# Kernel optimization log

Measured on AMD Instinct MI355X. Metric: run time of the kernel, lower is better.

## Reference

```python
import jax, jax.numpy as jnp
import numpy as np

B, I, O = 4096, 2048, 2048
U_R, THR_MIN = 0.01, 0.01


def setup_inputs() -> dict:
    key = jax.random.key(0)
    ks = jax.random.split(key, 4)
    # Random small-scale weights (the module's ones-init saturates sigmoids;
    # math is identical, this just keeps values in a testable range).
    return {
        "x_t": jax.random.normal(ks[0], (B, I), jnp.float32),
        "u_t": jnp.zeros((B, O), jnp.float32),
        "b_t": jnp.zeros((B, O), jnp.float32),
        "spk": jnp.zeros((B, O), jnp.float32),
        "W_syn": jax.random.normal(ks[1], (O, I), jnp.float32) * 0.02,
        "b_syn": jnp.zeros((O,), jnp.float32),
        "W_Tm": jax.random.normal(ks[2], (O, O), jnp.float32) * 0.02,
        "b_Tm": jnp.zeros((O,), jnp.float32),
        "W_Tadp": jax.random.normal(ks[3], (O, O), jnp.float32) * 0.02,
        "b_Tadp": jnp.zeros((O,), jnp.float32),
    }


def reference(x_t, u_t, b_t, spk, W_syn, b_syn, W_Tm, b_Tm, W_Tadp, b_Tadp):
    # L1 = syn(x_t); Linear stores weight [out,in]
    L1 = x_t @ W_syn.T + b_syn                      # [B, O]
    alpha = jax.nn.sigmoid((L1 + u_t) @ W_Tm.T + b_Tm)
    rho = jax.nn.sigmoid((L1 + b_t) @ W_Tadp.T + b_Tadp)
    b_new = rho * b_t + (1.0 - rho) * spk
    thr = THR_MIN + 1.8 * b_new
    u_new = u_t + (-u_t + L1) / alpha
    o_spk = (u_new - thr > 0).astype(jnp.float32)
    # (state u_t would be reset via o_spk, but forward returns only spikes)
    return o_spk
```

## Files before the change

### kernel.cpp

```cpp
#include <hip/hip_runtime.h>
#include <cmath>

#define B_DIM 4096
#define O_DIM 2048
#define I_DIM 2048

typedef _Float16 f16x8 __attribute__((ext_vector_type(8)));
typedef float f32x4 __attribute__((ext_vector_type(4)));
typedef unsigned int uint;
typedef unsigned short ushort;

#define WSCALE   64.0f
#define WDESCALE 0.015625f
#define MBYTE    ((size_t)1024 * 1024)


__device__ __forceinline__ int TP(int r, int s) {
    return r * 16 + (((s ^ ((r >> 1) & 3))) << 2);
}

__device__ __forceinline__ float h2f(ushort u) {
    _Float16 h = __builtin_bit_cast(_Float16, u);
    return (float)h;
}

__device__ __forceinline__ void gload16(const uint* src, uint* lds) {
    __builtin_amdgcn_global_load_lds(
        (const __attribute__((address_space(1))) void*)src,
        (__attribute__((address_space(3))) void*)lds, 16, 0, 0);
}

__device__ __forceinline__ void split8(const float4 a, const float4 b,
                                       uint4& hi, uint4& lo) {
    auto h0 = __builtin_amdgcn_cvt_pkrtz(a.x, a.y);
    auto h1 = __builtin_amdgcn_cvt_pkrtz(a.z, a.w);
    auto h2 = __builtin_amdgcn_cvt_pkrtz(b.x, b.y);
    auto h3 = __builtin_amdgcn_cvt_pkrtz(b.z, b.w);
    auto l0 = __builtin_amdgcn_cvt_pkrtz(a.x - (float)h0[0], a.y - (float)h0[1]);
    auto l1 = __builtin_amdgcn_cvt_pkrtz(a.z - (float)h1[0], a.w - (float)h1[1]);
    auto l2 = __builtin_amdgcn_cvt_pkrtz(b.x - (float)h2[0], b.y - (float)h2[1]);
    auto l3 = __builtin_amdgcn_cvt_pkrtz(b.z - (float)h3[0], b.w - (float)h3[1]);
    hi.x = __builtin_bit_cast(uint, h0); hi.y = __builtin_bit_cast(uint, h1);
    hi.z = __builtin_bit_cast(uint, h2); hi.w = __builtin_bit_cast(uint, h3);
    lo.x = __builtin_bit_cast(uint, l0); lo.y = __builtin_bit_cast(uint, l1);
    lo.z = __builtin_bit_cast(uint, l2); lo.w = __builtin_bit_cast(uint, l3);
}

__device__ __forceinline__ float4 add4(const float4 a, const float4 b) {
    return make_float4(a.x + b.x, a.y + b.y, a.z + b.z, a.w + b.w);
}
__device__ __forceinline__ float4 mul64(const float4 a) {
    return make_float4(a.x * WSCALE, a.y * WSCALE, a.z * WSCALE, a.w * WSCALE);
}
__device__ __forceinline__ void unpack8(const uint4 h, const uint4 l,
                                        float4& f0, float4& f1) {
    f0.x = h2f((ushort)(h.x & 0xffff)) + h2f((ushort)(l.x & 0xffff));
    f0.y = h2f((ushort)(h.x >> 16))    + h2f((ushort)(l.x >> 16));
    f0.z = h2f((ushort)(h.y & 0xffff)) + h2f((ushort)(l.y & 0xffff));
    f0.w = h2f((ushort)(h.y >> 16))    + h2f((ushort)(l.y >> 16));
    f1.x = h2f((ushort)(h.z & 0xffff)) + h2f((ushort)(l.z & 0xffff));
    f1.y = h2f((ushort)(h.z >> 16))    + h2f((ushort)(l.z >> 16));
    f1.z = h2f((ushort)(h.w & 0xffff)) + h2f((ushort)(l.w & 0xffff));
    f1.w = h2f((ushort)(h.w >> 16))    + h2f((ushort)(l.w >> 16));
}

__global__ __launch_bounds__(256)
void prep(const float* __restrict__ x, const float* __restrict__ Wsyn,
          const float* __restrict__ WTm,
          const float* __restrict__ u, const float* __restrict__ b,
          const float* __restrict__ s,
          ushort* __restrict__ Xh, ushort* __restrict__ Xl,
          ushort* __restrict__ Wsh, ushort* __restrict__ Wsl,
          ushort* __restrict__ Mhp, uint* __restrict__ flag, int doX) {
    const uint NX = (uint)((size_t)B_DIM * I_DIM / 8);
    const uint NW = (uint)((size_t)O_DIM * I_DIM / 8);
    const uint NZ = (uint)((size_t)B_DIM * O_DIM / 8);
    const uint nx = doX ? NX : 0;
    const uint total = nx + 2 * NW + NZ;
    const uint stride = gridDim.x * blockDim.x;
    bool nz = false;
    for (uint t = blockIdx.x * blockDim.x + threadIdx.x; t < total; t += stride) {
        if (t < nx) {
            const size_t i = (size_t)t * 8;
            uint4 h, l;
            split8(*(const float4*)(x + i), *(const float4*)(x + i + 4), h, l);
            *(uint4*)(Xh + i) = h; *(uint4*)(Xl + i) = l;
        } else if (t < nx + NW) {
            const size_t i = (size_t)(t - nx) * 8;
            uint4 h, l;
            split8(mul64(*(const float4*)(Wsyn + i)),
                   mul64(*(const float4*)(Wsyn + i + 4)), h, l);
            *(uint4*)(Wsh + i) = h; *(uint4*)(Wsl + i) = l;
        } else if (t < nx + 2 * NW) {
            const size_t i = (size_t)(t - nx - NW) * 8;
            const float4 a = mul64(*(const float4*)(WTm + i));
            const float4 c = mul64(*(const float4*)(WTm + i + 4));
            auto h0 = __builtin_amdgcn_cvt_pkrtz(a.x, a.y);
            auto h1 = __builtin_amdgcn_cvt_pkrtz(a.z, a.w);
            auto h2 = __builtin_amdgcn_cvt_pkrtz(c.x, c.y);
            auto h3 = __builtin_amdgcn_cvt_pkrtz(c.z, c.w);
            uint4 h;
            h.x = __builtin_bit_cast(uint, h0); h.y = __builtin_bit_cast(uint, h1);
            h.z = __builtin_bit_cast(uint, h2); h.w = __builtin_bit_cast(uint, h3);
            *(uint4*)(Mhp + i) = h;
        } else {
            const size_t i = (size_t)(t - nx - 2 * NW) * 8;
            const float4 a0 = *(const float4*)(u + i), a1 = *(const float4*)(u + i + 4);
            const float4 b0 = *(const float4*)(b + i), b1 = *(const float4*)(b + i + 4);
            const float4 c0 = *(const float4*)(s + i), c1 = *(const float4*)(s + i + 4);
            nz |= (a0.x != 0.f) | (a0.y != 0.f) | (a0.z != 0.f) | (a0.w != 0.f);
            nz |= (a1.x != 0.f) | (a1.y != 0.f) | (a1.z != 0.f) | (a1.w != 0.f);
            nz |= (b0.x != 0.f) | (b0.y != 0.f) | (b0.z != 0.f) | (b0.w != 0.f);
            nz |= (b1.x != 0.f) | (b1.y != 0.f) | (b1.z != 0.f) | (b1.w != 0.f);
            nz |= (c0.x != 0.f) | (c0.y != 0.f) | (c0.z != 0.f) | (c0.w != 0.f);
            nz |= (c1.x != 0.f) | (c1.y != 0.f) | (c1.z != 0.f) | (c1.w != 0.f);
        }
    }
    if (nz) atomicOr(flag, 1u);
}

__device__ __forceinline__ void gemm1_epilogue(
        f32x4 (&acc)[4][4], const float* bias, ushort* Lh, ushort* Ll,
        int row0, int col0, int lane, int wm, int wn) {
    const int fr = lane & 15;
#pragma unroll
    for (int ni = 0; ni < 4; ni++) {
        const int col = col0 + wn * 64 + ni * 16 + fr;
        const float bv = bias[col];
#pragma unroll
        for (int mi = 0; mi < 4; mi++) {
            const int rb = row0 + wm * 64 + mi * 16 + ((lane >> 4) << 2);
            float e[4];
#pragma unroll
            for (int r = 0; r < 4; r++) e[r] = acc[mi][ni][r] * WDESCALE + bv;
            auto hp0 = __builtin_amdgcn_cvt_pkrtz(e[0], e[1]);
            auto hp1 = __builtin_amdgcn_cvt_pkrtz(e[2], e[3]);
            auto lp0 = __builtin_amdgcn_cvt_pkrtz(e[0] - (float)hp0[0], e[1] - (float)hp0[1]);
            auto lp1 = __builtin_amdgcn_cvt_pkrtz(e[2] - (float)hp1[0], e[3] - (float)hp1[1]);
            const uint uh0 = __builtin_bit_cast(uint, hp0);
            const uint uh1 = __builtin_bit_cast(uint, hp1);
            const uint ul0 = __builtin_bit_cast(uint, lp0);
            const uint ul1 = __builtin_bit_cast(uint, lp1);
            Lh[(size_t)(rb + 0) * O_DIM + col] = (ushort)(uh0 & 0xffff);
            Lh[(size_t)(rb + 1) * O_DIM + col] = (ushort)(uh0 >> 16);
            Lh[(size_t)(rb + 2) * O_DIM + col] = (ushort)(uh1 & 0xffff);
            Lh[(size_t)(rb + 3) * O_DIM + col] = (ushort)(uh1 >> 16);
            Ll[(size_t)(rb + 0) * O_DIM + col] = (ushort)(ul0 & 0xffff);
            Ll[(size_t)(rb + 1) * O_DIM + col] = (ushort)(ul0 >> 16);
            Ll[(size_t)(rb + 2) * O_DIM + col] = (ushort)(ul1 & 0xffff);
            Ll[(size_t)(rb + 3) * O_DIM + col] = (ushort)(ul1 >> 16);
        }
    }
}

__global__ __launch_bounds__(256)
void gemm1_a(const ushort* __restrict__ Xh, const ushort* __restrict__ Xl,
             const ushort* __restrict__ Wh, const ushort* __restrict__ Wl,
             const float* __restrict__ bias,
             ushort* __restrict__ Lh, ushort* __restrict__ Ll) {
    __shared__ uint S[2][8192];

    const int tid = threadIdx.x;
    const int lane = tid & 63;
    const int wid = tid >> 6;
    const int wm = wid >> 1, wn = wid & 1;

    int sid = blockIdx.x;
    sid = (sid & 7) * 64 + (sid >> 3);
    const int bx = sid & 15, by = sid >> 4;
    const int row0 = by * 128, col0 = bx * 128;

    int r0, q0, r1, q1;
    {
        const int g0 = (wid * 2 + 0) * 64 + lane;
        const int g1 = (wid * 2 + 1) * 64 + lane;
        r0 = g0 >> 2; q0 = (g0 & 3) ^ ((r0 >> 1) & 3);
        r1 = g1 >> 2; q1 = (g1 & 3) ^ ((r1 >> 1) & 3);
    }
    const uint* sXh0 = (const uint*)Xh + (size_t)(row0 + r0) * 1024 + q0 * 4;
    const uint* sXh1 = (const uint*)Xh + (size_t)(row0 + r1) * 1024 + q1 * 4;
    const uint* sXl0 = (const uint*)Xl + (size_t)(row0 + r0) * 1024 + q0 * 4;
    const uint* sXl1 = (const uint*)Xl + (size_t)(row0 + r1) * 1024 + q1 * 4;
    const uint* sWh0 = (const uint*)Wh + (size_t)(col0 + r0) * 1024 + q0 * 4;
    const uint* sWh1 = (const uint*)Wh + (size_t)(col0 + r1) * 1024 + q1 * 4;
    const uint* sWl0 = (const uint*)Wl + (size_t)(col0 + r0) * 1024 + q0 * 4;
    const uint* sWl1 = (const uint*)Wl + (size_t)(col0 + r1) * 1024 + q1 * 4;
    const int c0 = (wid * 2 + 0) << 8;
    const int c1 = (wid * 2 + 1) << 8;

    f32x4 acc[4][4];
#pragma unroll
    for (int i = 0; i < 4; i++)
#pragma unroll
        for (int j = 0; j < 4; j++)
#pragma unroll
            for (int r = 0; r < 4; r++) acc[i][j][r] = 0.0f;

    const int fr = lane & 15;
    const int sl = lane >> 4;
    const int NT = I_DIM / 32;

    gload16(sXh0, &S[0][c0]);          gload16(sXh1, &S[0][c1]);
    gload16(sXl0, &S[0][2048 + c0]);   gload16(sXl1, &S[0][2048 + c1]);
    gload16(sWh0, &S[0][4096 + c0]);   gload16(sWh1, &S[0][4096 + c1]);
    gload16(sWl0, &S[0][6144 + c0]);   gload16(sWl1, &S[0][6144 + c1]);
    __syncthreads();

    int buf = 0;
    for (int t = 0; t < NT; t++) {
        if (t + 1 < NT) {
            const int ko = (t + 1) * 16;
            gload16(sXh0 + ko, &S[buf ^ 1][c0]);
            gload16(sXh1 + ko, &S[buf ^ 1][c1]);
            gload16(sXl0 + ko, &S[buf ^ 1][2048 + c0]);
            gload16(sXl1 + ko, &S[buf ^ 1][2048 + c1]);
            gload16(sWh0 + ko, &S[buf ^ 1][4096 + c0]);
            gload16(sWh1 + ko, &S[buf ^ 1][4096 + c1]);
            gload16(sWl0 + ko, &S[buf ^ 1][6144 + c0]);
            gload16(sWl1 + ko, &S[buf ^ 1][6144 + c1]);
        }
        f16x8 ah_[4], al_[4], bh_[4], bl_[4];
#pragma unroll
        for (int mi = 0; mi < 4; mi++) {
            const int r = wm * 64 + mi * 16 + fr;
            ah_[mi] = *(const f16x8*)&S[buf][TP(r, sl)];
            al_[mi] = *(const f16x8*)&S[buf][2048 + TP(r, sl)];
        }
#pragma unroll
        for (int ni = 0; ni < 4; ni++) {
            const int r = wn * 64 + ni * 16 + fr;
            bh_[ni] = *(const f16x8*)&S[buf][4096 + TP(r, sl)];
            bl_[ni] = *(const f16x8*)&S[buf][6144 + TP(r, sl)];
        }
#pragma unroll
        for (int mi = 0; mi < 4; mi++)
#pragma unroll
            for (int ni = 0; ni < 4; ni++) {
                acc[mi][ni] = __builtin_amdgcn_mfma_f32_16x16x32_f16(ah_[mi], bh_[ni], acc[mi][ni], 0, 0, 0);
                acc[mi][ni] = __builtin_amdgcn_mfma_f32_16x16x32_f16(ah_[mi], bl_[ni], acc[mi][ni], 0, 0, 0);
                acc[mi][ni] = __builtin_amdgcn_mfma_f32_16x16x32_f16(al_[mi], bh_[ni], acc[mi][ni], 0, 0, 0);
            }
        __syncthreads();
        buf ^= 1;
    }

    gemm1_epilogue(acc, bias, Lh, Ll, row0, col0, lane, wm, wn);
}

__global__ __launch_bounds__(256)
void gemm1_b(const float* __restrict__ X,
             const ushort* __restrict__ Wh, const ushort* __restrict__ Wl,
             const float* __restrict__ bias,
             ushort* __restrict__ Lh, ushort* __restrict__ Ll) {
    __shared__ uint S[8192];

    const int tid = threadIdx.x;
    const int lane = tid & 63;
    const int wid = tid >> 6;
    const int wm = wid >> 1, wn = wid & 1;

    int sid = blockIdx.x;
    sid = (sid & 7) * 64 + (sid >> 3);
    const int bx = sid & 15, by = sid >> 4;
    const int row0 = by * 128, col0 = bx * 128;

    const int sr = tid >> 1;
    const int kh = (tid & 1) * 16;
    const int s0 = (tid & 1) * 2;
    const float* pA = X + (size_t)(row0 + sr) * I_DIM + kh;

    int r0, q0, r1, q1;
    {
        const int g0 = (wid * 2 + 0) * 64 + lane;
        const int g1 = (wid * 2 + 1) * 64 + lane;
        r0 = g0 >> 2; q0 = (g0 & 3) ^ ((r0 >> 1) & 3);
        r1 = g1 >> 2; q1 = (g1 & 3) ^ ((r1 >> 1) & 3);
    }
    const uint* sWh0 = (const uint*)Wh + (size_t)(col0 + r0) * 1024 + q0 * 4;
    const uint* sWh1 = (const uint*)Wh + (size_t)(col0 + r1) * 1024 + q1 * 4;
    const uint* sWl0 = (const uint*)Wl + (size_t)(col0 + r0) * 1024 + q0 * 4;
    const uint* sWl1 = (const uint*)Wl + (size_t)(col0 + r1) * 1024 + q1 * 4;
    const int c0 = (wid * 2 + 0) << 8;
    const int c1 = (wid * 2 + 1) << 8;

    f32x4 acc[4][4];
#pragma unroll
    for (int i = 0; i < 4; i++)
#pragma unroll
        for (int j = 0; j < 4; j++)
#pragma unroll
            for (int r = 0; r < 4; r++) acc[i][j][r] = 0.0f;

    const int fr = lane & 15;
    const int sl = lane >> 4;
    const int NT = I_DIM / 32;

    float4 a0 = *(const float4*)(pA + 0), a1 = *(const float4*)(pA + 4);
    float4 a2 = *(const float4*)(pA + 8), a3 = *(const float4*)(pA + 12);
    uint4 xh0, xl0, xh1, xl1;
    split8(a0, a1, xh0, xl0);
    split8(a2, a3, xh1, xl1);

    for (int t = 0; t < NT; t++) {
        __syncthreads();
        *(uint4*)&S[TP(sr, s0)] = xh0;         *(uint4*)&S[TP(sr, s0 + 1)] = xh1;
        *(uint4*)&S[2048 + TP(sr, s0)] = xl0;  *(uint4*)&S[2048 + TP(sr, s0 + 1)] = xl1;
        const int ko = t * 16;
        gload16(sWh0 + ko, &S[4096 + c0]);  gload16(sWh1 + ko, &S[4096 + c1]);
        gload16(sWl0 + ko, &S[6144 + c0]);  gload16(sWl1 + ko, &S[6144 + c1]);
        __syncthreads();
        if (t + 1 < NT) {
            const float* nA = pA + (t + 1) * 32;
            a0 = *(const float4*)(nA + 0); a1 = *(const float4*)(nA + 4);
            a2 = *(const float4*)(nA + 8); a3 = *(const float4*)(nA + 12);
        }
        f16x8 ah_[4], al_[4], bh_[4], bl_[4];
#pragma unroll
        for (int mi = 0; mi < 4; mi++) {
            const int r = wm * 64 + mi * 16 + fr;
            ah_[mi] = *(const f16x8*)&S[TP(r, sl)];
            al_[mi] = *(const f16x8*)&S[2048 + TP(r, sl)];
        }
#pragma unroll
        for (int ni = 0; ni < 4; ni++) {
            const int r = wn * 64 + ni * 16 + fr;
            bh_[ni] = *(const f16x8*)&S[4096 + TP(r, sl)];
            bl_[ni] = *(const f16x8*)&S[6144 + TP(r, sl)];
        }
#pragma unroll
        for (int mi = 0; mi < 4; mi++)
#pragma unroll
            for (int ni = 0; ni < 4; ni++) {
                acc[mi][ni] = __builtin_amdgcn_mfma_f32_16x16x32_f16(ah_[mi], bh_[ni], acc[mi][ni], 0, 0, 0);
                acc[mi][ni] = __builtin_amdgcn_mfma_f32_16x16x32_f16(ah_[mi], bl_[ni], acc[mi][ni], 0, 0, 0);
                acc[mi][ni] = __builtin_amdgcn_mfma_f32_16x16x32_f16(al_[mi], bh_[ni], acc[mi][ni], 0, 0, 0);
            }
        if (t + 1 < NT) {
            split8(a0, a1, xh0, xl0);
            split8(a2, a3, xh1, xl1);
        }
    }

    gemm1_epilogue(acc, bias, Lh, Ll, row0, col0, lane, wm, wn);
}

__global__ __launch_bounds__(256)
void stage2_fast(const ushort* __restrict__ Lhp, const ushort* __restrict__ Llp,
                 const ushort* __restrict__ Mhp,
                 const float* __restrict__ bTm, float* __restrict__ out,
                 const uint* __restrict__ flag,
                 uint* __restrict__ cnt, uint* __restrict__ list, uint cap) {
    if (*flag != 0) return;

    __shared__ uint S[2][4096];

    const int tid = threadIdx.x;
    const int lane = tid & 63;
    const int wid = tid >> 6;
    const int wm = wid >> 1, wn = wid & 1;

    int sid = blockIdx.x;
    sid = (sid & 7) * 128 + (sid >> 3);
    const int bx = sid & 31, by = sid >> 5;
    const int row0 = by * 128, col0 = bx * 64;

    const uint* src[3];
    int base[3];
#pragma unroll
    for (int i = 0; i < 3; i++) {
        const int ch = wid * 3 + i;
        base[i] = ch << 8;
        if (ch < 8) {
            const int g = ch * 64 + lane;
            const int r = g >> 2, q = (g & 3) ^ ((r >> 1) & 3);
            src[i] = (const uint*)Lhp + (size_t)(row0 + r) * 1024 + q * 4;
        } else {
            const int g = (ch - 8) * 64 + lane;
            const int r = g >> 2, q = (g & 3) ^ ((r >> 1) & 3);
            src[i] = (const uint*)Mhp + (size_t)(col0 + r) * 1024 + q * 4;
        }
    }

    f32x4 acc[4][2];
#pragma unroll
    for (int i = 0; i < 4; i++)
#pragma unroll
        for (int j = 0; j < 2; j++)
#pragma unroll
            for (int r = 0; r < 4; r++) acc[i][j][r] = 0.0f;

    const int fr = lane & 15;
    const int sl = lane >> 4;
    const int NT = O_DIM / 32;

#pragma unroll
    for (int i = 0; i < 3; i++) gload16(src[i], &S[0][base[i]]);
    __syncthreads();

    int buf = 0;
    for (int t = 0; t < NT; t++) {
        if (t + 1 < NT) {
            const int ko = (t + 1) * 16;
#pragma unroll
            for (int i = 0; i < 3; i++) gload16(src[i] + ko, &S[buf ^ 1][base[i]]);
        }
        f16x8 lh_[4], mh_[2];
#pragma unroll
        for (int mi = 0; mi < 4; mi++)
            lh_[mi] = *(const f16x8*)&S[buf][TP(wm * 64 + mi * 16 + fr, sl)];
#pragma unroll
        for (int ni = 0; ni < 2; ni++)
            mh_[ni] = *(const f16x8*)&S[buf][2048 + TP(wn * 32 + ni * 16 + fr, sl)];
#pragma unroll
        for (int mi = 0; mi < 4; mi++)
#pragma unroll
            for (int ni = 0; ni < 2; ni++)
                acc[mi][ni] = __builtin_amdgcn_mfma_f32_16x16x32_f16(lh_[mi], mh_[ni], acc[mi][ni], 0, 0, 0);
        __syncthreads();
        buf ^= 1;
    }

    float* Sf = (float*)&S[0][0];
    float bmv[2];
#pragma unroll
    for (int ni = 0; ni < 2; ni++)
        bmv[ni] = bTm[col0 + wn * 32 + ni * 16 + fr];

#pragma unroll
    for (int ni = 0; ni < 2; ni++) {
#pragma unroll
        for (int mi = 0; mi < 4; mi++) {
            const int rbL = wm * 64 + mi * 16 + ((lane >> 4) << 2);
#pragma unroll
            for (int r = 0; r < 4; r++) {
                const int row = rbL + r;
                const int cm = wn * 32 + ni * 16 + fr;
                const int phys = (cm + ((row >> 2) & 3) * 16 + (row & 3) * 4) & 63;
                Sf[row * 64 + phys] = acc[mi][ni][r] * WDESCALE + bmv[ni];
            }
        }
    }
    __syncthreads();
    const int erow = tid >> 1;
    const int ecg  = tid & 1;
    const int rsw = ((erow >> 2) & 3) * 16 + (erow & 3) * 4;
    float z[32];
#pragma unroll
    for (int j = 0; j < 8; j++) {
        const int phys = (ecg * 32 + j * 4 + rsw) & 63;
        *(float4*)&z[j * 4] = *(const float4*)&Sf[erow * 64 + phys];
    }
    const int colBase = col0 + ecg * 32;
    const size_t idx0 = (size_t)(row0 + erow) * O_DIM + colBase;
    uint4 lh4[4], ll4[4];
#pragma unroll
    for (int j = 0; j < 4; j++) {
        lh4[j] = ((const uint4*)(Lhp + idx0))[j];
        ll4[j] = ((const uint4*)(Llp + idx0))[j];
    }
    float ov[32];
#pragma unroll
    for (int m = 0; m < 32; m++) {
        const uint hu = ((const uint*)lh4)[m >> 1];
        const uint lu = ((const uint*)ll4)[m >> 1];
        const ushort hs = (m & 1) ? (ushort)(hu >> 16) : (ushort)(hu & 0xffff);
        const ushort ls = (m & 1) ? (ushort)(lu >> 16) : (ushort)(lu & 0xffff);
        const float l1 = h2f(hs) + h2f(ls);
        const float zm = z[m];
        const float ea = expf(-zm);
        const float d = l1 * (1.0f + ea) - 0.01f;
        ov[m] = d > 0.0f ? 1.0f : 0.0f;
        const float tol = 2e-4f + 1e-4f * ea * (1.0f + fabsf(l1));
        if (fabsf(d) < tol) {
            const uint pos = atomicAdd(cnt, 1u);
            if (pos < cap) list[pos] = (uint)(idx0 + m);
        }
    }
#pragma unroll
    for (int j = 0; j < 8; j++)
        *(float4*)(out + idx0 + j * 4) = *(const float4*)&ov[j * 4];
}

__global__ __launch_bounds__(512)
void stage2_slow(const ushort* __restrict__ Lhp, const ushort* __restrict__ Llp,
                 const float* __restrict__ u_t, const float* __restrict__ b_t,
                 const float* __restrict__ spk,
                 const float* __restrict__ WTm, const float* __restrict__ bTm,
                 const float* __restrict__ WTa, const float* __restrict__ bTa,
                 float* __restrict__ out, const uint* __restrict__ flag,
                 uint* __restrict__ cnt, uint* __restrict__ list, uint cap) {
    if (*flag == 0) return;

    __shared__ uint A1h[128][20], A1l[128][20], A2h[128][20], A2l[128][20];
    __shared__ uint Mh[128][20],  Ml[128][20],  Gh[128][20],  Gl[128][20];

    const int tid = threadIdx.x;
    const int lane = tid & 63;
    const int wid = tid >> 6;
    const int wm = wid >> 2;
    const int wn = wid & 3;

    int sid = blockIdx.x;
    sid = (sid & 7) * 64 + (sid >> 3);
    const int bx = sid & 15, by = sid >> 4;
    const int row0 = by * 128, col0 = bx * 128;

    const int srow = tid >> 2;
    const int skb = (tid & 3) * 8;
    const int swc = (tid & 3) * 4;

    const size_t aoff = (size_t)(row0 + srow) * O_DIM + skb;
    const float* pU = u_t + aoff;
    const float* pT = b_t + aoff;
    const float* pM = WTm + (size_t)(col0 + srow) * O_DIM + skb;
    const float* pG = WTa + (size_t)(col0 + srow) * O_DIM + skb;

    f32x4 accM[4][2], accA[4][2];
#pragma unroll
    for (int i = 0; i < 4; i++)
#pragma unroll
        for (int j = 0; j < 2; j++)
#pragma unroll
            for (int r = 0; r < 4; r++) { accM[i][j][r] = 0.0f; accA[i][j][r] = 0.0f; }

    float4 lq0, lq1;
    {
        const uint4 LH = *(const uint4*)(Lhp + aoff);
        const uint4 LL = *(const uint4*)(Llp + aoff);
        unpack8(LH, LL, lq0, lq1);
    }
    float4 uq0 = *(const float4*)(pU + 0), uq1 = *(const float4*)(pU + 4);
    float4 tq0 = *(const float4*)(pT + 0), tq1 = *(const float4*)(pT + 4);
    float4 mq0 = *(const float4*)(pM + 0), mq1 = *(const float4*)(pM + 4);
    float4 gq0 = *(const float4*)(pG + 0), gq1 = *(const float4*)(pG + 4);

    const int fr = lane & 15;
    const int kq = (lane >> 4) * 4;

    for (int t = 0; t < O_DIM / 32; t++) {
        uint4 A1hi, A1lo, A2hi, A2lo, Mhi, Mlo, Ghi, Glo;
        split8(add4(lq0, uq0), add4(lq1, uq1), A1hi, A1lo);
        split8(add4(lq0, tq0), add4(lq1, tq1), A2hi, A2lo);
        split8(mul64(mq0), mul64(mq1), Mhi, Mlo);
        split8(mul64(gq0), mul64(gq1), Ghi, Glo);
        __syncthreads();
        *(uint4*)&A1h[srow][swc] = A1hi;  *(uint4*)&A1l[srow][swc] = A1lo;
        *(uint4*)&A2h[srow][swc] = A2hi;  *(uint4*)&A2l[srow][swc] = A2lo;
        *(uint4*)&Mh[srow][swc]  = Mhi;   *(uint4*)&Ml[srow][swc]  = Mlo;
        *(uint4*)&Gh[srow][swc]  = Ghi;   *(uint4*)&Gl[srow][swc]  = Glo;
        __syncthreads();
        if (t + 1 < O_DIM / 32) {
            const int o = (t + 1) * 32;
            const uint4 LH = *(const uint4*)(Lhp + aoff + o);
            const uint4 LL = *(const uint4*)(Llp + aoff + o);
            unpack8(LH, LL, lq0, lq1);
            uq0 = *(const float4*)(pU + o);  uq1 = *(const float4*)(pU + o + 4);
            tq0 = *(const float4*)(pT + o);  tq1 = *(const float4*)(pT + o + 4);
            mq0 = *(const float4*)(pM + o);  mq1 = *(const float4*)(pM + o + 4);
            gq0 = *(const float4*)(pG + o);  gq1 = *(const float4*)(pG + o + 4);
        }
        {
            f16x8 ah_[4], al_[4], bh_[2], bl_[2];
#pragma unroll
            for (int mi = 0; mi < 4; mi++) {
                const int r = wm * 64 + mi * 16 + fr;
                ah_[mi] = *(const f16x8*)&A1h[r][kq];
                al_[mi] = *(const f16x8*)&A1l[r][kq];
            }
#pragma unroll
            for (int ni = 0; ni < 2; ni++) {
                const int r = wn * 32 + ni * 16 + fr;
                bh_[ni] = *(const f16x8*)&Mh[r][kq];
                bl_[ni] = *(const f16x8*)&Ml[r][kq];
            }
#pragma unroll
            for (int mi = 0; mi < 4; mi++)
#pragma unroll
                for (int ni = 0; ni < 2; ni++) {
                    accM[mi][ni] = __builtin_amdgcn_mfma_f32_16x16x32_f16(ah_[mi], bh_[ni], accM[mi][ni], 0, 0, 0);
                    accM[mi][ni] = __builtin_amdgcn_mfma_f32_16x16x32_f16(ah_[mi], bl_[ni], accM[mi][ni], 0, 0, 0);
                    accM[mi][ni] = __builtin_amdgcn_mfma_f32_16x16x32_f16(al_[mi], bh_[ni], accM[mi][ni], 0, 0, 0);
                }
        }
        {
            f16x8 ah_[4], al_[4], bh_[2], bl_[2];
#pragma unroll
            for (int mi = 0; mi < 4; mi++) {
                const int r = wm * 64 + mi * 16 + fr;
                ah_[mi] = *(const f16x8*)&A2h[r][kq];
                al_[mi] = *(const f16x8*)&A2l[r][kq];
            }
#pragma unroll
            for (int ni = 0; ni < 2; ni++) {
                const int r = wn * 32 + ni * 16 + fr;
                bh_[ni] = *(const f16x8*)&Gh[r][kq];
                bl_[ni] = *(const f16x8*)&Gl[r][kq];
            }
#pragma unroll
            for (int mi = 0; mi < 4; mi++)
#pragma unroll
                for (int ni = 0; ni < 2; ni++) {
                    accA[mi][ni] = __builtin_amdgcn_mfma_f32_16x16x32_f16(ah_[mi], bh_[ni], accA[mi][ni], 0, 0, 0);
                    accA[mi][ni] = __builtin_amdgcn_mfma_f32_16x16x32_f16(ah_[mi], bl_[ni], accA[mi][ni], 0, 0, 0);
                    accA[mi][ni] = __builtin_amdgcn_mfma_f32_16x16x32_f16(al_[mi], bh_[ni], accA[mi][ni], 0, 0, 0);
                }
        }
    }

#pragma unroll
    for (int ni = 0; ni < 2; ni++) {
        const int col = col0 + wn * 32 + ni * 16 + fr;
        const float bm = bTm[col], bg = bTa[col];
#pragma unroll
        for (int mi = 0; mi < 4; mi++) {
            const int rb = row0 + wm * 64 + mi * 16 + ((lane >> 4) << 2);
#pragma unroll
            for (int r = 0; r < 4; r++) {
                const size_t idx = (size_t)(rb + r) * O_DIM + col;
                const float zm = accM[mi][ni][r] * WDESCALE + bm;
                const float za = accA[mi][ni][r] * WDESCALE + bg;
                const float ut = u_t[idx], bt = b_t[idx];
                const float sp = spk[idx];
                const float l1 = h2f(Lhp[idx]) + h2f(Llp[idx]);
                const float ea  = expf(-zm);
                const float rho = 1.0f / (1.0f + expf(-za));
                const float bn  = sp + rho * (bt - sp);
                const float thr = 0.01f + 1.8f * bn;
                const float un  = ut + (l1 - ut) * (1.0f + ea);
                const float d   = un - thr;
                out[idx] = d > 0.0f ? 1.0f : 0.0f;
                const float tol = 2e-4f + 1e-4f * ea * (1.0f + fabsf(l1 - ut))
                                + 2e-4f * fabsf(bt - sp);
                if (fabsf(d) < tol) {
                    const uint pos = atomicAdd(cnt, 1u);
                    if (pos < cap) list[pos] = (uint)idx;
                }
            }
        }
    }
}

__global__ __launch_bounds__(256)
void lsnn_fixup(const ushort* __restrict__ Lhp, const ushort* __restrict__ Llp,
                const float* __restrict__ X, const float* __restrict__ Wsyn,
                const float* __restrict__ bsyn,
                const float* __restrict__ u_t, const float* __restrict__ b_t,
                const float* __restrict__ spk,
                const float* __restrict__ WTm, const float* __restrict__ bTm,
                const float* __restrict__ WTa, const float* __restrict__ bTa,
                const uint* __restrict__ cnt, const uint* __restrict__ list,
                uint cap, float* __restrict__ out) {
    const uint nc = *cnt;
    const uint n = nc < cap ? nc : cap;
    const int lane = threadIdx.x & 63;
    const uint wid = (blockIdx.x * blockDim.x + threadIdx.x) >> 6;
    const uint nw = (gridDim.x * blockDim.x) >> 6;

    for (uint e = wid; e < n; e += nw) {
        const uint idx = list[e];
        const int b = idx >> 11;
        const int o = idx & (O_DIM - 1);

        double l1 = 0.0, zm = 0.0, za = 0.0;
        const float* xr = X + (size_t)b * I_DIM;
        const float* wr = Wsyn + (size_t)o * I_DIM;
        for (int k = lane; k < I_DIM; k += 64)
            l1 = fma((double)xr[k], (double)wr[k], l1);

        const ushort* lhr = Lhp + (size_t)b * O_DIM;
        const ushort* llr = Llp + (size_t)b * O_DIM;
        const float* ur = u_t + (size_t)b * O_DIM;
        const float* tr = b_t + (size_t)b * O_DIM;
        const float* mr = WTm + (size_t)o * O_DIM;
        const float* ar = WTa + (size_t)o * O_DIM;
        for (int k = lane; k < O_DIM; k += 64) {
            const double l = (double)(h2f(lhr[k]) + h2f(llr[k]));
            zm = fma(l + (double)ur[k], (double)mr[k], zm);
            za = fma(l + (double)tr[k], (double)ar[k], za);
        }
#pragma unroll
        for (int off = 32; off > 0; off >>= 1) {
            l1 += __shfl_down(l1, off);
            zm += __shfl_down(zm, off);
            za += __shfl_down(za, off);
        }
        if (lane == 0) {
            l1 += (double)bsyn[o];
            zm += (double)bTm[o];
            za += (double)bTa[o];
            const double inv_alpha = 1.0 + exp(-zm);
            const double rho = 1.0 / (1.0 + exp(-za));
            const double bt = (double)b_t[idx];
            const double sp = (double)spk[idx];
            const double ut = (double)u_t[idx];
            const double b_new = sp + rho * (bt - sp);
            const double thr = 0.01 + 1.8 * b_new;
            const double u_new = ut + (l1 - ut) * inv_alpha;
            out[idx] = (u_new - thr > 0.0) ? 1.0f : 0.0f;
        }
    }
}

extern "C" void kernel_launch(void* const* d_in, const int* in_sizes, int n_in,
                              void* d_out, int out_size, void* d_ws, size_t ws_size,
                              hipStream_t stream) {
    const float* x    = (const float*)d_in[0];
    const float* u_t  = (const float*)d_in[1];
    const float* b_t  = (const float*)d_in[2];
    const float* spk  = (const float*)d_in[3];
    const float* Wsyn = (const float*)d_in[4];
    const float* bsyn = (const float*)d_in[5];
    const float* WTm  = (const float*)d_in[6];
    const float* bTm  = (const float*)d_in[7];
    const float* WTa  = (const float*)d_in[8];
    const float* bTa  = (const float*)d_in[9];
    float* out = (float*)d_out;

    char* ws = (char*)d_ws;
    ushort* Lhp = (ushort*)(ws + 0 * MBYTE);
    ushort* Llp = (ushort*)(ws + 16 * MBYTE);
    ushort* Mhp = (ushort*)(ws + 32 * MBYTE);
    ushort* Wsh = (ushort*)(ws + 40 * MBYTE);
    ushort* Wsl = (ushort*)(ws + 48 * MBYTE);

    const bool tierA = ws_size >= 91 * MBYTE;
    const size_t flag_off = tierA ? 88 * MBYTE : 56 * MBYTE;
    if (ws_size < flag_off + (1u << 16)) return;

    ushort* Xh = (ushort*)(ws + 56 * MBYTE);
    ushort* Xl = (ushort*)(ws + 72 * MBYTE);
    uint* flag = (uint*)(ws + flag_off);
    uint* cnt  = (uint*)(ws + flag_off + 4);
    uint* list = (uint*)(ws + flag_off + 256);
    const uint cap = (uint)((ws_size - flag_off - 256) / sizeof(uint));

    (void)hipMemsetAsync(ws + flag_off, 0, 8, stream);
    prep<<<dim3(2048), dim3(256), 0, stream>>>(x, Wsyn, WTm, u_t, b_t, spk,
                                               Xh, Xl, Wsh, Wsl, Mhp, flag,
                                               tierA ? 1 : 0);
    if (tierA) {
        gemm1_a<<<dim3(512), dim3(256), 0, stream>>>(Xh, Xl, Wsh, Wsl, bsyn, Lhp, Llp);
    } else {
        gemm1_b<<<dim3(512), dim3(256), 0, stream>>>(x, Wsh, Wsl, bsyn, Lhp, Llp);
    }
    stage2_fast<<<dim3(1024), dim3(256), 0, stream>>>(Lhp, Llp, Mhp, bTm,
                                                      out, flag, cnt, list, cap);
    stage2_slow<<<dim3(512), dim3(512), 0, stream>>>(Lhp, Llp, u_t, b_t, spk,
                                                     WTm, bTm, WTa, bTa,
                                                     out, flag, cnt, list, cap);
    lsnn_fixup<<<dim3(256), dim3(256), 0, stream>>>(Lhp, Llp, x, Wsyn, bsyn,
                                                    u_t, b_t, spk,
                                                    WTm, bTm, WTa, bTa,
                                                    cnt, list, cap, out);
}
```

Measured before the change: 277.9 us.

## Replace first-stage GEMM with 8-wave triple-buffered LDS pipeline kernel

Adds gemm1_c, which uses 512 threads (8 waves, each owning a 64x32 sub-tile) and a three-slot LDS ring. Loads are prefetched two K-steps ahead, and explicit s_waitcnt/s_barrier replace the per-iteration __syncthreads. The goal is to hide global-to-LDS latency behind the split-fp16 MFMA work and raise wave-level parallelism per block. The cost is 96KB of LDS per block, which limits occupancy, plus hand-counted vmcnt waits that depend on each gload16 being a single memory op. The shared epilogue helper is inlined into gemm1_b, and gemm1_a is removed.

```diff
diff --git a/kernel.cpp b/kernel.cpp
--- a/kernel.cpp
+++ b/kernel.cpp
@@ -119,13 +119,95 @@
     if (nz) atomicOr(flag, 1u);
 }
 
-__device__ __forceinline__ void gemm1_epilogue(
-        f32x4 (&acc)[4][4], const float* bias, ushort* Lh, ushort* Ll,
-        int row0, int col0, int lane, int wm, int wn) {
+__global__ __launch_bounds__(512)
+void gemm1_c(const ushort* __restrict__ Xh, const ushort* __restrict__ Xl,
+             const ushort* __restrict__ Wh, const ushort* __restrict__ Wl,
+             const float* __restrict__ bias,
+             ushort* __restrict__ Lh, ushort* __restrict__ Ll) {
+    __shared__ uint S[3][8192];
+
+    const int tid = threadIdx.x;
+    const int lane = tid & 63;
+    const int wid = tid >> 6;
+    const int wm = wid >> 2;
+    const int wn = wid & 3;
+
+    int sid = blockIdx.x;
+    sid = (sid & 7) * 64 + (sid >> 3);
+    const int bx = sid & 15, by = sid >> 4;
+    const int row0 = by * 128, col0 = bx * 128;
+
+    const uint* src[4];
+    int dbase[4];
+#pragma unroll
+    for (int i = 0; i < 4; i++) {
+        const int ch = wid * 4 + i;
+        const int p = ch >> 3, c = ch & 7;
+        const int g = c * 64 + lane;
+        const int r = g >> 2, q = (g & 3) ^ ((r >> 1) & 3);
+        dbase[i] = p * 2048 + c * 256;
+        const ushort* plane = (p == 0) ? Xh : (p == 1) ? Xl : (p == 2) ? Wh : Wl;
+        const int grow = (p < 2) ? (row0 + r) : (col0 + r);
+        src[i] = (const uint*)plane + (size_t)grow * 1024 + q * 4;
+    }
+
+    f32x4 acc[4][2];
+#pragma unroll
+    for (int i = 0; i < 4; i++)
+#pragma unroll
+        for (int j = 0; j < 2; j++)
+#pragma unroll
+            for (int r = 0; r < 4; r++) acc[i][j][r] = 0.0f;
+
     const int fr = lane & 15;
-#pragma unroll
-    for (int ni = 0; ni < 4; ni++) {
-        const int col = col0 + wn * 64 + ni * 16 + fr;
+    const int sl = lane >> 4;
+    const int NT = I_DIM / 32;
+
+#pragma unroll
+    for (int i = 0; i < 4; i++) gload16(src[i], &S[0][dbase[i]]);
+#pragma unroll
+    for (int i = 0; i < 4; i++) gload16(src[i] + 16, &S[1][dbase[i]]);
+
+    for (int t = 0; t < NT; t++) {
+        if (t + 1 < NT) {
+            asm volatile("s_waitcnt vmcnt(4)" ::: "memory");
+        } else {
+            asm volatile("s_waitcnt vmcnt(0)" ::: "memory");
+        }
+        asm volatile("s_barrier" ::: "memory");
+        if (t + 2 < NT) {
+            const int ko = (t + 2) * 16;
+            uint* Sd = &S[(t + 2) % 3][0];
+#pragma unroll
+            for (int i = 0; i < 4; i++) gload16(src[i] + ko, &Sd[dbase[i]]);
+        }
+        const uint* Sc = &S[t % 3][0];
+        f16x8 ah_[4], al_[4], bh_[2], bl_[2];
+#pragma unroll
+        for (int mi = 0; mi < 4; mi++) {
+            const int r = wm * 64 + mi * 16 + fr;
+            ah_[mi] = *(const f16x8*)&Sc[TP(r, sl)];
+            al_[mi] = *(const f16x8*)&Sc[2048 + TP(r, sl)];
+        }
+#pragma unroll
+        for (int ni = 0; ni < 2; ni++) {
+            const int r = wn * 32 + ni * 16 + fr;
+            bh_[ni] = *(const f16x8*)&Sc[4096 + TP(r, sl)];
+            bl_[ni] = *(const f16x8*)&Sc[6144 + TP(r, sl)];
+        }
+#pragma unroll
+        for (int mi = 0; mi < 4; mi++)
+#pragma unroll
+            for (int ni = 0; ni < 2; ni++) {
+                acc[mi][ni] = __builtin_amdgcn_mfma_f32_16x16x32_f16(ah_[mi], bh_[ni], acc[mi][ni], 0, 0, 0);
+                acc[mi][ni] = __builtin_amdgcn_mfma_f32_16x16x32_f16(ah_[mi], bl_[ni], acc[mi][ni], 0, 0, 0);
+                acc[mi][ni] = __builtin_amdgcn_mfma_f32_16x16x32_f16(al_[mi], bh_[ni], acc[mi][ni], 0, 0, 0);
+            }
+    }
+
+#pragma unroll
+    for (int ni = 0; ni < 2; ni++) {
+        const int col = col0 + wn * 32 + ni * 16 + fr;
         const float bv = bias[col];
 #pragma unroll
         for (int mi = 0; mi < 4; mi++) {
@@ -154,100 +236,6 @@
 }
 
 __global__ __launch_bounds__(256)
-void gemm1_a(const ushort* __restrict__ Xh, const ushort* __restrict__ Xl,
-             const ushort* __restrict__ Wh, const ushort* __restrict__ Wl,
-             const float* __restrict__ bias,
-             ushort* __restrict__ Lh, ushort* __restrict__ Ll) {
-    __shared__ uint S[2][8192];
-
-    const int tid = threadIdx.x;
-    const int lane = tid & 63;
-    const int wid = tid >> 6;
-    const int wm = wid >> 1, wn = wid & 1;
-
-    int sid = blockIdx.x;
-    sid = (sid & 7) * 64 + (sid >> 3);
-    const int bx = sid & 15, by = sid >> 4;
-    const int row0 = by * 128, col0 = bx * 128;
-
-    int r0, q0, r1, q1;
-    {
-        const int g0 = (wid * 2 + 0) * 64 + lane;
-        const int g1 = (wid * 2 + 1) * 64 + lane;
-        r0 = g0 >> 2; q0 = (g0 & 3) ^ ((r0 >> 1) & 3);
-        r1 = g1 >> 2; q1 = (g1 & 3) ^ ((r1 >> 1) & 3);
-    }
-    const uint* sXh0 = (const uint*)Xh + (size_t)(row0 + r0) * 1024 + q0 * 4;
-    const uint* sXh1 = (const uint*)Xh + (size_t)(row0 + r1) * 1024 + q1 * 4;
-    const uint* sXl0 = (const uint*)Xl + (size_t)(row0 + r0) * 1024 + q0 * 4;
-    const uint* sXl1 = (const uint*)Xl + (size_t)(row0 + r1) * 1024 + q1 * 4;
-    const uint* sWh0 = (const uint*)Wh + (size_t)(col0 + r0) * 1024 + q0 * 4;
-    const uint* sWh1 = (const uint*)Wh + (size_t)(col0 + r1) * 1024 + q1 * 4;
-    const uint* sWl0 = (const uint*)Wl + (size_t)(col0 + r0) * 1024 + q0 * 4;
-    const uint* sWl1 = (const uint*)Wl + (size_t)(col0 + r1) * 1024 + q1 * 4;
-    const int c0 = (wid * 2 + 0) << 8;
-    const int c1 = (wid * 2 + 1) << 8;
-
-    f32x4 acc[4][4];
-#pragma unroll
-    for (int i = 0; i < 4; i++)
-#pragma unroll
-        for (int j = 0; j < 4; j++)
-#pragma unroll
-            for (int r = 0; r < 4; r++) acc[i][j][r] = 0.0f;
-
-    const int fr = lane & 15;
-    const int sl = lane >> 4;
-    const int NT = I_DIM / 32;
-
-    gload16(sXh0, &S[0][c0]);          gload16(sXh1, &S[0][c1]);
-    gload16(sXl0, &S[0][2048 + c0]);   gload16(sXl1, &S[0][2048 + c1]);
-    gload16(sWh0, &S[0][4096 + c0]);   gload16(sWh1, &S[0][4096 + c1]);
-    gload16(sWl0, &S[0][6144 + c0]);   gload16(sWl1, &S[0][6144 + c1]);
-    __syncthreads();
-
-    int buf = 0;
-    for (int t = 0; t < NT; t++) {
-        if (t + 1 < NT) {
-            const int ko = (t + 1) * 16;
-            gload16(sXh0 + ko, &S[buf ^ 1][c0]);
-            gload16(sXh1 + ko, &S[buf ^ 1][c1]);
-            gload16(sXl0 + ko, &S[buf ^ 1][2048 + c0]);
-            gload16(sXl1 + ko, &S[buf ^ 1][2048 + c1]);
-            gload16(sWh0 + ko, &S[buf ^ 1][4096 + c0]);
-            gload16(sWh1 + ko, &S[buf ^ 1][4096 + c1]);
-            gload16(sWl0 + ko, &S[buf ^ 1][6144 + c0]);
-            gload16(sWl1 + ko, &S[buf ^ 1][6144 + c1]);
-        }
-        f16x8 ah_[4], al_[4], bh_[4], bl_[4];
-#pragma unroll
-        for (int mi = 0; mi < 4; mi++) {
-            const int r = wm * 64 + mi * 16 + fr;
-            ah_[mi] = *(const f16x8*)&S[buf][TP(r, sl)];
-            al_[mi] = *(const f16x8*)&S[buf][2048 + TP(r, sl)];
-        }
-#pragma unroll
-        for (int ni = 0; ni < 4; ni++) {
-            const int r = wn * 64 + ni * 16 + fr;
-            bh_[ni] = *(const f16x8*)&S[buf][4096 + TP(r, sl)];
-            bl_[ni] = *(const f16x8*)&S[buf][6144 + TP(r, sl)];
-        }
-#pragma unroll
-        for (int mi = 0; mi < 4; mi++)
-#pragma unroll
-            for (int ni = 0; ni < 4; ni++) {
-                acc[mi][ni] = __builtin_amdgcn_mfma_f32_16x16x32_f16(ah_[mi], bh_[ni], acc[mi][ni], 0, 0, 0);
-                acc[mi][ni] = __builtin_amdgcn_mfma_f32_16x16x32_f16(ah_[mi], bl_[ni], acc[mi][ni], 0, 0, 0);
-                acc[mi][ni] = __builtin_amdgcn_mfma_f32_16x16x32_f16(al_[mi], bh_[ni], acc[mi][ni], 0, 0, 0);
-            }
-        __syncthreads();
-        buf ^= 1;
-    }
-
-    gemm1_epilogue(acc, bias, Lh, Ll, row0, col0, lane, wm, wn);
-}
-
-__global__ __launch_bounds__(256)
 void gemm1_b(const float* __restrict__ X,
              const ushort* __restrict__ Wh, const ushort* __restrict__ Wl,
              const float* __restrict__ bias,
@@ -341,7 +329,35 @@
         }
     }
 
-    gemm1_epilogue(acc, bias, Lh, Ll, row0, col0, lane, wm, wn);
+    const int fr2 = lane & 15;
+#pragma unroll
+    for (int ni = 0; ni < 4; ni++) {
+        const int col = col0 + wn * 64 + ni * 16 + fr2;
+        const float bv = bias[col];
+#pragma unroll
+        for (int mi = 0; mi < 4; mi++) {
+            const int rb = row0 + wm * 64 + mi * 16 + ((lane >> 4) << 2);
+            float e[4];
+#pragma unroll
+            for (int r = 0; r < 4; r++) e[r] = acc[mi][ni][r] * WDESCALE + bv;
+            auto hp0 = __builtin_amdgcn_cvt_pkrtz(e[0], e[1]);
+            auto hp1 = __builtin_amdgcn_cvt_pkrtz(e[2], e[3]);
+            auto lp0 = __builtin_amdgcn_cvt_pkrtz(e[0] - (float)hp0[0], e[1] - (float)hp0[1]);
+            auto lp1 = __builtin_amdgcn_cvt_pkrtz(e[2] - (float)hp1[0], e[3] - (float)hp1[1]);
+            const uint uh0 = __builtin_bit_cast(uint, hp0);
+            const uint uh1 = __builtin_bit_cast(uint, hp1);
+            const uint ul0 = __builtin_bit_cast(uint, lp0);
+            const uint ul1 = __builtin_bit_cast(uint, lp1);
+            Lh[(size_t)(rb + 0) * O_DIM + col] = (ushort)(uh0 & 0xffff);
+            Lh[(size_t)(rb + 1) * O_DIM + col] = (ushort)(uh0 >> 16);
+            Lh[(size_t)(rb + 2) * O_DIM + col] = (ushort)(uh1 & 0xffff);
+            Lh[(size_t)(rb + 3) * O_DIM + col] = (ushort)(uh1 >> 16);
+            Ll[(size_t)(rb + 0) * O_DIM + col] = (ushort)(ul0 & 0xffff);
+            Ll[(size_t)(rb + 1) * O_DIM + col] = (ushort)(ul0 >> 16);
+            Ll[(size_t)(rb + 2) * O_DIM + col] = (ushort)(ul1 & 0xffff);
+            Ll[(size_t)(rb + 3) * O_DIM + col] = (ushort)(ul1 >> 16);
+        }
+    }
 }
 
 __global__ __launch_bounds__(256)
@@ -739,7 +755,7 @@
                                                Xh, Xl, Wsh, Wsl, Mhp, flag,
                                                tierA ? 1 : 0);
     if (tierA) {
-        gemm1_a<<<dim3(512), dim3(256), 0, stream>>>(Xh, Xl, Wsh, Wsl, bsyn, Lhp, Llp);
+        gemm1_c<<<dim3(512), dim3(512), 0, stream>>>(Xh, Xl, Wsh, Wsl, bsyn, Lhp, Llp);
     } else {
         gemm1_b<<<dim3(512), dim3(256), 0, stream>>>(x, Wsh, Wsl, bsyn, Lhp, Llp);
     }
```

After: 266.0 us. -4.3%, faster.
